# Kernel tuning notes

Measured on AMD Instinct MI355X. Metric: run time of the kernel, lower is better.

The kernel has to match this reference:

```python
import jax, jax.numpy as jnp
import numpy as np

B, S, HID = 2, 2048, 2048
NH, NKV, D = 32, 8, 64
M = 256          # FAVOR+ random features
CHUNK = 128      # causal chunk size
EPS = 1e-6


def setup_inputs():
    key = jax.random.key(0)
    ks = jax.random.split(key, 7)
    hidden_states = jax.random.normal(ks[0], (B, S, HID), jnp.float32)
    # RoPE tables (HF Llama style): [B, S, D]
    inv_freq = 1.0 / (10000.0 ** (jnp.arange(0, D, 2, dtype=jnp.float32) / D))
    freqs = jnp.arange(S, dtype=jnp.float32)[:, None] * inv_freq[None, :]   # [S, D/2]
    emb = jnp.concatenate([freqs, freqs], axis=-1)                          # [S, D]
    cos = jnp.broadcast_to(jnp.cos(emb)[None], (B, S, D)).astype(jnp.float32)
    sin = jnp.broadcast_to(jnp.sin(emb)[None], (B, S, D)).astype(jnp.float32)
    sc = 0.02
    Wq = jax.random.normal(ks[1], (NH * D, HID), jnp.float32) * sc
    Wk = jax.random.normal(ks[2], (NKV * D, HID), jnp.float32) * sc
    Wv = jax.random.normal(ks[3], (NKV * D, HID), jnp.float32) * sc
    Wo = jax.random.normal(ks[4], (HID, NH * D), jnp.float32) * sc
    proj = jax.random.normal(ks[5], (M, D), jnp.float32)  # FAVOR+ random projection
    return {"hidden_states": hidden_states, "cos": cos, "sin": sin,
            "Wq": Wq, "Wk": Wk, "Wv": Wv, "Wo": Wo, "proj": proj}


def rotate_half(x):
    x1, x2 = x[..., : x.shape[-1] // 2], x[..., x.shape[-1] // 2:]
    return jnp.concatenate([-x2, x1], axis=-1)


def favor_features(x, proj, is_query):
    # FAVOR+ positive softmax-kernel features: phi(x) = exp(Wx' - |x'|^2/2 - stab)/sqrt(m)
    dn = x.shape[-1] ** -0.25
    xn = x * dn                                            # data normalizer d^{-1/4}
    xp = jnp.einsum('bhsd,md->bhsm', xn, proj)             # [B,H,S,M]
    sq = 0.5 * jnp.sum(xn * xn, axis=-1, keepdims=True)
    if is_query:
        stab = jnp.max(xp, axis=-1, keepdims=True)
    else:
        stab = jnp.max(xp, axis=(-1, -2), keepdims=True)
    return (jnp.exp(xp - sq - stab) + EPS) / jnp.sqrt(jnp.asarray(M, xp.dtype))


def causal_linear_attention(phi_q, phi_k, v):
    # phi_q/phi_k: [B,H,S,M], v: [B,H,S,D]; causal chunked prefix formulation
    Bh, H, T, m = phi_q.shape
    d = v.shape[-1]
    nc = T // CHUNK
    qc = phi_q.reshape(Bh, H, nc, CHUNK, m)
    kc = phi_k.reshape(Bh, H, nc, CHUNK, m)
    vc = v.reshape(Bh, H, nc, CHUNK, d)
    # per-chunk KV state and key sums
    kv = jnp.einsum('bhscm,bhscd->bhsmd', kc, vc)          # [B,H,nc,M,D]
    kz = jnp.sum(kc, axis=3)                               # [B,H,nc,M]
    kv_pre = jnp.cumsum(kv, axis=2) - kv                   # exclusive prefix
    kz_pre = jnp.cumsum(kz, axis=2) - kz
    inter = jnp.einsum('bhscm,bhsmd->bhscd', qc, kv_pre)
    inter_z = jnp.einsum('bhscm,bhsm->bhsc', qc, kz_pre)
    # intra-chunk causal part
    mask = jnp.tril(jnp.ones((CHUNK, CHUNK), phi_q.dtype))
    scores = jnp.einsum('bhscm,bhstm->bhsct', qc, kc) * mask
    intra = jnp.einsum('bhsct,bhstd->bhscd', scores, vc)
    intra_z = jnp.sum(scores, axis=-1)
    out = (inter + intra) / (inter_z + intra_z + EPS)[..., None]
    return out.reshape(Bh, H, T, d)


def reference(hidden_states, cos, sin, Wq, Wk, Wv, Wo, proj):
    b, s, _ = hidden_states.shape
    q = (hidden_states @ Wq.T).reshape(b, s, NH, D).transpose(0, 2, 1, 3)   # [B,NH,S,D]
    k = (hidden_states @ Wk.T).reshape(b, s, NKV, D).transpose(0, 2, 1, 3)  # [B,NKV,S,D]
    v = (hidden_states @ Wv.T).reshape(b, s, NKV, D).transpose(0, 2, 1, 3)
    c, si = cos[:, None, :, :], sin[:, None, :, :]
    q = q * c + rotate_half(q) * si
    k = k * c + rotate_half(k) * si
    groups = NH // NKV
    k = jnp.repeat(k, groups, axis=1)
    v = jnp.repeat(v, groups, axis=1)
    phi_q = favor_features(q, proj, is_query=True)
    phi_k = favor_features(k, proj, is_query=False)
    attn = causal_linear_attention(phi_q, phi_k, v)                         # [B,NH,S,D]
    attn = attn.transpose(0, 2, 1, 3).reshape(b, s, NH * D)
    return attn @ Wo.T
```

## Files before the change

kernel.cpp:

```cpp
#include <hip/hip_runtime.h>
#include <hip/hip_bf16.h>

#define SEQ   2048
#define NHEAD 32
#define NKVH  8
#define DH    64
#define MFEAT 256
#define NCH   16
#define EPSF  1e-6f

typedef __hip_bfloat16 bf16;
typedef unsigned short u16;
typedef __attribute__((ext_vector_type(8))) short short8;
typedef __attribute__((ext_vector_type(4))) float f32x4;

__device__ __forceinline__ float b2f(bf16 x){ return __bfloat162float(x); }
__device__ __forceinline__ bf16  f2b(float x){ return __float2bfloat16(x); }
__device__ __forceinline__ u16   f2u(float x){ bf16 h = __float2bfloat16(x); return *reinterpret_cast<u16*>(&h); }

__device__ __forceinline__ bool probe_f32(const unsigned* __restrict__ p){
  return (p[0] & 0xFFFFu) == 0u;
}
__device__ __forceinline__ float loadIn(const void* __restrict__ ptr, size_t idx, bool f32){
  return f32 ? ((const float*)ptr)[idx] : b2f(((const bf16*)ptr)[idx]);
}

__device__ __forceinline__ void cp16(u16* lds, const u16* g){
  __builtin_amdgcn_global_load_lds((const __attribute__((address_space(1))) unsigned*)g,
      (__attribute__((address_space(3))) unsigned*)lds, 16, 0, 0);
}

#define MFMA16(a,b,c) __builtin_amdgcn_mfma_f32_16x16x32_bf16(a,b,c,0,0,0)
#define SBAR()  do { __builtin_amdgcn_s_barrier(); __builtin_amdgcn_sched_barrier(0); } while(0)

__global__ __launch_bounds__(256) void conv_kernel(const void* __restrict__ src,
    u16* __restrict__ dst, const unsigned* __restrict__ probe)
{
  const bool f32in = probe_f32(probe);
  size_t i = (size_t)blockIdx.x*256 + threadIdx.x;
  if (f32in){
    const float4* s = (const float4*)src;
    float4 a = s[i*2], b = s[i*2+1];
    u16 t[8] = {f2u(a.x),f2u(a.y),f2u(a.z),f2u(a.w),
                f2u(b.x),f2u(b.y),f2u(b.z),f2u(b.w)};
    *(short8*)&dst[i*8] = *(const short8*)t;
  } else {
    ((short8*)dst)[i] = ((const short8*)src)[i];
  }
}

__global__ __launch_bounds__(512) void gemm_mfma(const u16* __restrict__ A,
    const u16* __restrict__ W, float* __restrict__ oq, float* __restrict__ ok,
    float* __restrict__ ov, void* __restrict__ outAny, int K, int N, int mode,
    const void* __restrict__ cosg, const void* __restrict__ sing,
    const unsigned* __restrict__ probe)
{
  __shared__ __align__(16) u16 sA[3][16384];
  __shared__ __align__(16) u16 sB[3][8192];
  const int tid = threadIdx.x;
  const int lane = tid & 63, wave = tid >> 6;

  const int nbx = gridDim.x;
  const int nwg = nbx * gridDim.y;
  int id = blockIdx.y * nbx + blockIdx.x;
  int sw = id;
  if ((nwg & 7) == 0) sw = (id & 7) * (nwg >> 3) + (id >> 3);
  const int bx = sw % nbx, by = sw / nbx;
  const int c0 = bx*128, r0 = by*256;

  const int wm = wave >> 1, wn = wave & 1;
  f32x4 acc[4][4] = {};

  const int rl  = lane >> 3;
  const int swzE = ((lane & 7) ^ rl) << 3;
  const u16* gA = A + (size_t)(r0 + wave*8 + rl)*K + swzE;
  const u16* gB = W + (size_t)(c0 + wave*8 + rl)*K + swzE;
  const int aDst = wave*512;
  const int bDst = wave*512;

  const int rowA = (wm*64 + (lane&15))*64;
  const int rowB = (wn*64 + (lane&15))*64;
  const int colS = (((lane>>4)*8) ^ ((lane&7)<<3));

  const int nk = K >> 6;

  #define STAGE_ALL(buf, t) do { const int k0_ = (t)*64;                  \
    cp16(&sA[buf][aDst],         gA + k0_);                               \
    cp16(&sA[buf][aDst + 4096],  gA + (size_t)64*K  + k0_);               \
    cp16(&sA[buf][aDst + 8192],  gA + (size_t)128*K + k0_);               \
    cp16(&sA[buf][aDst + 12288], gA + (size_t)192*K + k0_);               \
    cp16(&sB[buf][bDst],         gB + k0_);                               \
    cp16(&sB[buf][bDst + 4096],  gB + (size_t)64*K  + k0_); } while(0)

  STAGE_ALL(0, 0);
  STAGE_ALL(1, 1);

  int cur = 0;
  for (int t = 0; t < nk; ++t) {
    if (t < nk-1) asm volatile("s_waitcnt vmcnt(6)" ::: "memory");
    else          asm volatile("s_waitcnt vmcnt(0)" ::: "memory");
    SBAR();

    int sb = cur + 2; if (sb >= 3) sb -= 3;
    const int k0s = (t + 2) * 64;
    const bool st = (t + 2 < nk);
    const u16* bA_ = sA[cur];
    const u16* bB_ = sB[cur];

    short8 a01[2][2], a23[2][2], b01[2][2], b23[2][2];

    #pragma unroll
    for (int mt=0;mt<2;++mt){
      a01[mt][0] = *(const short8*)(bA_ + rowA + mt*1024 + colS);
      a01[mt][1] = *(const short8*)(bA_ + rowA + mt*1024 + (colS^32));
    }
    #pragma unroll
    for (int nt=0;nt<2;++nt){
      b01[nt][0] = *(const short8*)(bB_ + rowB + nt*1024 + colS);
      b01[nt][1] = *(const short8*)(bB_ + rowB + nt*1024 + (colS^32));
    }
    if (st){ cp16(&sA[sb][aDst], gA + k0s);
             cp16(&sA[sb][aDst + 4096], gA + (size_t)64*K + k0s); }
    SBAR();
    __builtin_amdgcn_s_setprio(1);
    #pragma unroll
    for (int mt=0;mt<2;++mt)
      #pragma unroll
      for (int nt=0;nt<2;++nt){
        acc[mt][nt] = MFMA16(a01[mt][0], b01[nt][0], acc[mt][nt]);
        acc[mt][nt] = MFMA16(a01[mt][1], b01[nt][1], acc[mt][nt]);
      }
    __builtin_amdgcn_s_setprio(0);
    SBAR();

    #pragma unroll
    for (int nt=0;nt<2;++nt){
      b23[nt][0] = *(const short8*)(bB_ + rowB + (nt+2)*1024 + colS);
      b23[nt][1] = *(const short8*)(bB_ + rowB + (nt+2)*1024 + (colS^32));
    }
    if (st){ cp16(&sA[sb][aDst + 8192],  gA + (size_t)128*K + k0s);
             cp16(&sA[sb][aDst + 12288], gA + (size_t)192*K + k0s); }
    SBAR();
    __builtin_amdgcn_s_setprio(1);
    #pragma unroll
    for (int mt=0;mt<2;++mt)
      #pragma unroll
      for (int nt=0;nt<2;++nt){
        acc[mt][nt+2] = MFMA16(a01[mt][0], b23[nt][0], acc[mt][nt+2]);
        acc[mt][nt+2] = MFMA16(a01[mt][1], b23[nt][1], acc[mt][nt+2]);
      }
    __builtin_amdgcn_s_setprio(0);
    SBAR();

    #pragma unroll
    for (int mt=0;mt<2;++mt){
      a23[mt][0] = *(const short8*)(bA_ + rowA + (mt+2)*1024 + colS);
      a23[mt][1] = *(const short8*)(bA_ + rowA + (mt+2)*1024 + (colS^32));
    }
    if (st){ cp16(&sB[sb][bDst], gB + k0s);
             cp16(&sB[sb][bDst + 4096], gB + (size_t)64*K + k0s); }
    SBAR();
    __builtin_amdgcn_s_setprio(1);
    #pragma unroll
    for (int mt=0;mt<2;++mt)
      #pragma unroll
      for (int nt=0;nt<2;++nt){
        acc[mt+2][nt+2] = MFMA16(a23[mt][0], b23[nt][0], acc[mt+2][nt+2]);
        acc[mt+2][nt+2] = MFMA16(a23[mt][1], b23[nt][1], acc[mt+2][nt+2]);
      }
    __builtin_amdgcn_s_setprio(0);
    SBAR();

    __builtin_amdgcn_s_setprio(1);
    #pragma unroll
    for (int mt=0;mt<2;++mt)
      #pragma unroll
      for (int nt=0;nt<2;++nt){
        acc[mt+2][nt] = MFMA16(a23[mt][0], b01[nt][0], acc[mt+2][nt]);
        acc[mt+2][nt] = MFMA16(a23[mt][1], b01[nt][1], acc[mt+2][nt]);
      }
    __builtin_amdgcn_s_setprio(0);

    cur = (cur == 2) ? 0 : cur + 1;
  }
  #undef STAGE_ALL

  const int rbase = r0 + wm*64 + (lane>>4)*4;
  const int cbase = c0 + wn*64 + (lane&15);
  if (mode == 0) {
    const bool f32o = probe_f32(probe);
    #pragma unroll
    for (int mt=0;mt<4;++mt)
      #pragma unroll
      for (int nt=0;nt<4;++nt)
        #pragma unroll
        for (int rg=0;rg<4;++rg){
          int r = rbase + mt*16 + rg, c = cbase + nt*16;
          float v = acc[mt][nt][rg];
          if (f32o) ((float*)outAny)[(size_t)r*N + c] = v;
          else      ((u16*)outAny)[(size_t)r*N + c] = f2u(v);
        }
  } else {
    const bool f32in = probe_f32(probe);
    const float dn = 0.3535533905932738f;
    #pragma unroll
    for (int nt=0;nt<4;++nt){
      int cc = cbase + nt*16;
      float* dst; int H2, cl; bool isv = false;
      if (cc < 2048){ dst = oq; H2 = 32; cl = cc; }
      else if (cc < 2560){ dst = ok; H2 = 8; cl = cc - 2048; }
      else { dst = ov; H2 = 8; cl = cc - 2560; isv = true; }
      int hh = cl>>6, dd = cl&63;
      float sgn = (dd < 32) ? -1.f : 1.f;
      #pragma unroll
      for (int mt=0;mt<4;++mt)
        #pragma unroll
        for (int rg=0;rg<4;++rg){
          int r = rbase + mt*16 + rg;
          int bb = r>>11, s = r&2047;
          float v = acc[mt][nt][rg];
          if (!isv){
            float vp = acc[mt][nt^2][rg];
            size_t ci = ((size_t)bb*SEQ + s)*DH + dd;
            float cv = loadIn(cosg, ci, f32in);
            float sv = loadIn(sing, ci, f32in);
            v = (v*cv + sgn*vp*sv) * dn;
          }
          dst[(((size_t)bb*H2 + hh)*SEQ + s)*DH + dd] = v;
        }
    }
  }
}

__global__ __launch_bounds__(256) void phi_mfma(const float* __restrict__ xn,
    const u16* __restrict__ projb, float* __restrict__ rmaxk,
    const float* __restrict__ stabk, u16* __restrict__ phi, int mode)
{
  __shared__ __align__(16) u16 sA[64*80];
  __shared__ __align__(16) u16 sP[256*80];
  __shared__ float sq[64];
  const int tid = threadIdx.x, lane = tid & 63, wave = tid >> 6;
  const size_t row0 = (size_t)blockIdx.x * 64;

  #pragma unroll
  for (int l = 0; l < 8; ++l){
    int v8 = tid + l*256;
    int off = v8*8; int m = off>>6, d = off&63;
    *(short8*)&sP[m*80 + d] = ((const short8*)projb)[v8];
  }
  {
    int r = tid >> 2, qq = tid & 3;
    const float* src = xn + (row0 + r)*DH + qq*16;
    float s = 0.f;
    u16 tmp[16];
    #pragma unroll
    for (int i=0;i<16;i+=4){
      float4 v4 = *(const float4*)&src[i];
      s += v4.x*v4.x + v4.y*v4.y + v4.z*v4.z + v4.w*v4.w;
      tmp[i] = f2u(v4.x); tmp[i+1] = f2u(v4.y); tmp[i+2] = f2u(v4.z); tmp[i+3] = f2u(v4.w);
    }
    *(short8*)&sA[r*80 + qq*16]     = *(short8*)&tmp[0];
    *(short8*)&sA[r*80 + qq*16 + 8] = *(short8*)&tmp[8];
    s += __shfl_xor(s, 1, 64);
    s += __shfl_xor(s, 2, 64);
    if (qq == 0) sq[r] = 0.5f*s;
  }
  __syncthreads();

  f32x4 acc[16] = {};
  const u16* pA = &sA[(wave*16 + (lane&15))*80 + (lane>>4)*8];
  short8 af0 = *(const short8*)(pA);
  short8 af1 = *(const short8*)(pA + 32);
  #pragma unroll
  for (int nt=0; nt<16; ++nt){
    const u16* pB = &sP[(nt*16 + (lane&15))*80 + (lane>>4)*8];
    short8 b0 = *(const short8*)(pB);
    short8 b1 = *(const short8*)(pB + 32);
    acc[nt] = MFMA16(af0, b0, acc[nt]);
    acc[nt] = MFMA16(af1, b1, acc[nt]);
  }

  float mx[4];
  #pragma unroll
  for (int rg=0; rg<4; ++rg){
    float m = acc[0][rg];
    #pragma unroll
    for (int nt=1; nt<16; ++nt) m = fmaxf(m, acc[nt][rg]);
    m = fmaxf(m, __shfl_xor(m, 1, 64));
    m = fmaxf(m, __shfl_xor(m, 2, 64));
    m = fmaxf(m, __shfl_xor(m, 4, 64));
    m = fmaxf(m, __shfl_xor(m, 8, 64));
    mx[rg] = m;
  }
  const int rloc = wave*16 + (lane>>4)*4;
  if (mode == 1){
    if ((lane & 15) == 0){
      #pragma unroll
      for (int rg=0;rg<4;++rg) rmaxk[row0 + rloc + rg] = mx[rg];
    }
    return;
  }
  float stab[4];
  if (mode == 0){
    #pragma unroll
    for (int rg=0;rg<4;++rg) stab[rg] = mx[rg];
  } else {
    float s = stabk[row0 >> 11];
    #pragma unroll
    for (int rg=0;rg<4;++rg) stab[rg] = s;
  }
  float sqr[4];
  #pragma unroll
  for (int rg=0;rg<4;++rg) sqr[rg] = sq[rloc + rg];
  #pragma unroll
  for (int nt=0;nt<16;++nt){
    #pragma unroll
    for (int rg=0;rg<4;++rg){
      float val = (__expf(fminf(acc[nt][rg] - sqr[rg] - stab[rg], 0.f)) + EPSF) * 0.0625f;
      phi[(row0 + rloc + rg)*MFEAT + nt*16 + (lane&15)] = f2u(val);
    }
  }
}

__global__ void stab_reduce_kernel(const float* __restrict__ rmaxk, float* __restrict__ stabk){
  __shared__ float red[256];
  int bk = blockIdx.x;
  float mx = -1e30f;
  for (int i = threadIdx.x; i < SEQ; i += 256) mx = fmaxf(mx, rmaxk[(size_t)bk*SEQ + i]);
  red[threadIdx.x] = mx; __syncthreads();
  for (int off=128; off>0; off>>=1){
    if ((int)threadIdx.x < off) red[threadIdx.x] = fmaxf(red[threadIdx.x], red[threadIdx.x+off]);
    __syncthreads();
  }
  if (threadIdx.x==0) stabk[bk] = red[0];
}

__global__ __launch_bounds__(256) void vtrans_kernel(const float* __restrict__ vbuf,
                                                     u16* __restrict__ vT)
{
  int blk = blockIdx.x;
  int bk = blk >> 4, sc = blk & 15;
  const float* src = vbuf + ((size_t)bk*SEQ + sc*128)*DH;
  __shared__ float sT[128*65];
  for (int i=0;i<32;++i){ int idx = threadIdx.x + i*256; sT[(idx>>6)*65 + (idx&63)] = src[idx]; }
  __syncthreads();
  #pragma unroll
  for (int i=0;i<4;++i){
    int gi = threadIdx.x + i*256;
    int d = gi >> 4, t8 = (gi & 15)*8;
    u16 tmp[8];
    #pragma unroll
    for (int j=0;j<8;++j) tmp[j] = f2u(sT[(t8+j)*65 + d]);
    *(short8*)&vT[((size_t)bk*DH + d)*SEQ + sc*128 + t8] = *(const short8*)tmp;
  }
}

__global__ __launch_bounds__(256) void kvchunk_kernel(const bf16* __restrict__ phik,
    const float* __restrict__ vbuf, float* __restrict__ kv, float* __restrict__ kz)
{
  int blk = blockIdx.x; int bk = blk >> 4, c = blk & 15;
  const bf16* Kc = phik + ((size_t)bk*SEQ + c*128)*MFEAT;
  const float* Vc = vbuf + ((size_t)bk*SEQ + c*128)*DH;
  __shared__ float sV[128*64];
  for (int l=0;l<32;++l){ int idx = threadIdx.x + l*256; sV[idx] = Vc[idx]; }
  __syncthreads();
  int m = threadIdx.x;
  float acc[64] = {}; float az = 0.f;
  for (int t=0;t<128;++t){
    float ph = b2f(Kc[(size_t)t*MFEAT + m]);
    az += ph;
    const float4* vr = (const float4*)&sV[t*64];
    #pragma unroll
    for (int d4=0; d4<16; ++d4){
      float4 v4 = vr[d4];
      acc[d4*4+0] += ph*v4.x; acc[d4*4+1] += ph*v4.y;
      acc[d4*4+2] += ph*v4.z; acc[d4*4+3] += ph*v4.w;
    }
  }
  float* out = kv + (size_t)blk*MFEAT*DH;
  #pragma unroll
  for (int d=0; d<64; ++d) out[(size_t)d*MFEAT + m] = acc[d];
  kz[(size_t)blk*MFEAT + m] = az;
}

__global__ void scan_kernel(float* __restrict__ p, u16* __restrict__ ob,
                            int inner, int nc, int total){
  int t = blockIdx.x*256 + threadIdx.x;
  if (t >= total) return;
  int outer = t / inner, rem = t - outer*inner;
  const float* base = p + (size_t)outer*nc*inner + rem;
  u16* obase = ob + (size_t)outer*nc*inner + rem;
  float run = 0.f;
  for (int c=0;c<nc;++c){
    float v = base[(size_t)c*inner];
    obase[(size_t)c*inner] = f2u(run);
    run += v;
  }
}

__global__ __launch_bounds__(256) void attn_mfma(
    const u16* __restrict__ phiq, const u16* __restrict__ phik,
    const u16* __restrict__ kvpb, const u16* __restrict__ kzpb,
    const u16* __restrict__ vT, u16* __restrict__ attnout)
{
  __shared__ __align__(16) u16 smem[27648];
  __shared__ float sZ[128];
  const int tid = threadIdx.x, lane = tid & 63, wave = tid >> 6;
  const int blk = blockIdx.x;
  const int c = blk & 15, h = (blk >> 4) & 31, b = blk >> 9;
  const int kvh = h >> 2;
  const int bkv = b*NKVH + kvh;
  const u16* Q   = phiq + (((size_t)(b*NHEAD+h)*SEQ) + c*128)*MFEAT;
  const u16* Kc  = phik + (((size_t)bkv*SEQ) + c*128)*MFEAT;
  const u16* KVb = kvpb + ((size_t)(bkv*NCH + c))*MFEAT*DH;
  const u16* KZb = kzpb + ((size_t)(bkv*NCH + c))*MFEAT;
  const u16* vTb = vT + (size_t)bkv*DH*SEQ;

  u16* sQ   = smem;
  u16* sK   = smem + 4096;
  u16* sKVT = smem + 8192;
  u16* sP   = smem;
  u16* sVT  = smem + 17408;

  f32x4 accS[2][8] = {};
  f32x4 accO[2][5] = {};

  #pragma unroll
  for (int i=0;i<4;++i){
    int gi = tid + i*256;
    int d  = gi >> 4, g = gi & 15;
    cp16(&sVT[(i*256 + wave*64)*8],
         vTb + (size_t)d*SEQ + c*128 + ((g ^ (d&7))<<3));
  }

  const int ch0 = wave*64 + lane, ch1 = 256 + wave*64 + lane;
  const u16* gQ0 = Q  + (ch0>>2)*MFEAT + (ch0&3)*8;
  const u16* gQ1 = Q  + (ch1>>2)*MFEAT + (ch1&3)*8;
  const u16* gK0 = Kc + (ch0>>2)*MFEAT + (ch0&3)*8;
  const u16* gK1 = Kc + (ch1>>2)*MFEAT + (ch1&3)*8;
  u16* lQ0 = &sQ[(wave*64)*8];  u16* lQ1 = &sQ[(256+wave*64)*8];
  u16* lK0 = &sK[(wave*64)*8];  u16* lK1 = &sK[(256+wave*64)*8];

  const int dKV = wave*16 + (lane>>2);
  const u16* gKVsrc = KVb + (size_t)dKV*MFEAT + (((lane&3) ^ (dKV&3))<<3);

  for (int k0 = 0; k0 < MFEAT; k0 += 32) {
    cp16(lQ0, gQ0 + k0); cp16(lQ1, gQ1 + k0);
    cp16(lK0, gK0 + k0); cp16(lK1, gK1 + k0);
    cp16(&sKVT[wave*512], gKVsrc + k0);
    if (tid < 4) cp16(&sKVT[2048], KZb + k0 + tid*8);
    __syncthreads();
    short8 af0, af1;
    const u16* pQ = &sQ[(wave*32 + (lane&15))*32 + (lane>>4)*8];
    af0 = *(const short8*)(pQ);
    af1 = *(const short8*)(pQ + 512);
    #pragma unroll
    for (int nt=0;nt<8;++nt){
      short8 bk = *(const short8*)&sK[(nt*16 + (lane&15))*32 + (lane>>4)*8];
      accS[0][nt] = MFMA16(af0, bk, accS[0][nt]);
      accS[1][nt] = MFMA16(af1, bk, accS[1][nt]);
    }
    #pragma unroll
    for (int nt=0;nt<5;++nt){
      int row = nt*16 + (lane&15);
      short8 bi = *(const short8*)&sKVT[row*32 + (((lane>>4) ^ (row&3))<<3)];
      accO[0][nt] = MFMA16(af0, bi, accO[0][nt]);
      accO[1][nt] = MFMA16(af1, bi, accO[1][nt]);
    }
    __syncthreads();
  }

  #pragma unroll
  for (int mt=0;mt<2;++mt){
    int rowb = wave*32 + mt*16 + (lane>>4)*4;
    #pragma unroll
    for (int nt=0;nt<8;++nt){
      int col = nt*16 + (lane&15);
      #pragma unroll
      for (int rg=0;rg<4;++rg){
        int row = rowb + rg;
        float v = (col <= row) ? accS[mt][nt][rg] : 0.f;
        sP[row*136 + col] = f2u(v);
      }
    }
  }
  if (tid < 16){
    u16 ones[8] = {0x3F80,0x3F80,0x3F80,0x3F80,0x3F80,0x3F80,0x3F80,0x3F80};
    *(short8*)&sVT[64*128 + tid*8] = *(const short8*)ones;
  }
  __syncthreads();

  #pragma unroll
  for (int kc=0;kc<4;++kc){
    const u16* pP = &sP[(wave*32 + (lane&15))*136 + kc*32 + (lane>>4)*8];
    short8 pa0 = *(const short8*)(pP);
    short8 pa1 = *(const short8*)(pP + 16*136);
    #pragma unroll
    for (int nt=0;nt<5;++nt){
      int row = nt*16 + (lane&15);
      int g   = kc*4 + (lane>>4);
      short8 bv = *(const short8*)&sVT[row*128 + ((g ^ (row&7))<<3)];
      accO[0][nt] = MFMA16(pa0, bv, accO[0][nt]);
      accO[1][nt] = MFMA16(pa1, bv, accO[1][nt]);
    }
  }

  if ((lane & 15) == 0){
    #pragma unroll
    for (int mt=0;mt<2;++mt){
      int rowb = wave*32 + mt*16 + (lane>>4)*4;
      #pragma unroll
      for (int rg=0;rg<4;++rg) sZ[rowb + rg] = accO[mt][4][rg];
    }
  }
  __syncthreads();
  const int d0 = lane & 15;
  #pragma unroll
  for (int mt=0;mt<2;++mt){
    int rowb = wave*32 + mt*16 + (lane>>4)*4;
    #pragma unroll
    for (int rg=0;rg<4;++rg){
      int row = rowb + rg;
      float inv = 1.0f / (sZ[row] + EPSF);
      int sg = c*128 + row;
      size_t ob = (((size_t)b*SEQ + sg)*NHEAD + h)*DH;
      #pragma unroll
      for (int nt=0;nt<4;++nt)
        attnout[ob + nt*16 + d0] = f2u(accO[mt][nt][rg] * inv);
    }
  }
}

extern "C" void kernel_launch(void* const* d_in, const int* in_sizes, int n_in,
                              void* d_out, int out_size, void* d_ws, size_t ws_size,
                              hipStream_t stream)
{
  const void* hidden = d_in[0];
  const void* cosg   = d_in[1];
  const void* sing   = d_in[2];
  const void* Wq     = d_in[3];
  const void* Wk     = d_in[4];
  const void* Wv     = d_in[5];
  const void* Wo     = d_in[6];
  const void* proj   = d_in[7];
  const unsigned* probe = (const unsigned*)d_in[1];

  float* ws = (float*)d_ws;
  float* xnq   = ws;
  float* kv    = ws;
  float* kz    = ws + 4194304;
  float* rmaxk = ws + 4259840;
  float* stabk = ws + 4292608;
  u16*   vT    = (u16*) (ws + 4292864);
  u16*   kvpb  = (u16*) (ws + 5341440);
  u16*   kzpb  = (u16*) (ws + 7438592);
  float* xnk   = ws + 8388608;
  float* vbuf  = ws + 10485760;
  u16*   projb = (u16*) (ws + 12582912);
  bf16*  phiq  = (bf16*)(ws + 12591104);
  bf16*  phik  = (bf16*)(ws + 29368320);
  u16*   hb    = (u16*) (ws + 33562624);
  u16*   attn  = (u16*) (ws + 33562624);
  u16*   wqkv  = (u16*) (ws + 37756928);
  u16*   wob   = (u16*) (ws + 37756928);

  conv_kernel<<<4096, 256, 0, stream>>>(hidden, hb, probe);
  conv_kernel<<<2048, 256, 0, stream>>>(Wq, wqkv,           probe);
  conv_kernel<<<512,  256, 0, stream>>>(Wk, wqkv + 4194304, probe);
  conv_kernel<<<512,  256, 0, stream>>>(Wv, wqkv + 5242880, probe);
  conv_kernel<<<8,    256, 0, stream>>>(proj, projb, probe);

  gemm_mfma<<<dim3(24,16), 512, 0, stream>>>(hb, wqkv, xnq, xnk, vbuf, nullptr,
                                             2048, 3072, 1, cosg, sing, probe);
  conv_kernel<<<2048, 256, 0, stream>>>(Wo, wob, probe);

  phi_mfma<<<2048, 256, 0, stream>>>(xnq, projb, nullptr, nullptr, (u16*)phiq, 0);
  vtrans_kernel<<<256, 256, 0, stream>>>(vbuf, vT);
  phi_mfma<<<512,  256, 0, stream>>>(xnk, projb, rmaxk, nullptr, nullptr, 1);
  stab_reduce_kernel<<<16, 256, 0, stream>>>(rmaxk, stabk);
  phi_mfma<<<512,  256, 0, stream>>>(xnk, projb, nullptr, stabk, (u16*)phik, 2);

  kvchunk_kernel<<<256, 256, 0, stream>>>(phik, vbuf, kv, kz);
  scan_kernel<<<1024, 256, 0, stream>>>(kv, kvpb, MFEAT*DH, NCH, 16*MFEAT*DH);
  scan_kernel<<<16,   256, 0, stream>>>(kz, kzpb, MFEAT,    NCH, 16*MFEAT);

  attn_mfma<<<1024, 256, 0, stream>>>((const u16*)phiq, (const u16*)phik,
                                      kvpb, kzpb, vT, attn);

  gemm_mfma<<<dim3(16,16), 512, 0, stream>>>(attn, wob, nullptr, nullptr, nullptr,
                                             d_out, 2048, 2048, 0, nullptr, nullptr, probe);
}
```

Baseline: 441.7 us.

## Double-buffer attention operand loads and coalesce feature-map stores via LDS

The attention kernel now double-buffers the Q, K and KV/KZ shared-memory tiles. The next 32-wide slice is prefetched with async copies while MFMAs run on the current slice, using explicit vmcnt waits and one barrier per step. Separately, the FAVOR feature kernel stages its exp outputs in a swizzled shared buffer and writes them to global memory as 16-byte coalesced vectors instead of scattered 2-byte stores. This raises LDS use per block, which may lower occupancy, and adds extra barriers to the feature kernel.

```diff
diff --git a/kernel.cpp b/kernel.cpp
--- a/kernel.cpp
+++ b/kernel.cpp
@@ -312,13 +312,27 @@
   float sqr[4];
   #pragma unroll
   for (int rg=0;rg<4;++rg) sqr[rg] = sq[rloc + rg];
+
+  __syncthreads();
+  u16* sOut = sP;
+  const int xorW = (lane>>4) << 2;
   #pragma unroll
   for (int nt=0;nt<16;++nt){
+    int gcol = nt*2 + ((lane&15)>>3);
+    int gS = (gcol ^ xorW)*8 + (lane&7);
     #pragma unroll
     for (int rg=0;rg<4;++rg){
       float val = (__expf(fminf(acc[nt][rg] - sqr[rg] - stab[rg], 0.f)) + EPSF) * 0.0625f;
-      phi[(row0 + rloc + rg)*MFEAT + nt*16 + (lane&15)] = f2u(val);
-    }
+      sOut[(rloc + rg)*256 + gS] = f2u(val);
+    }
+  }
+  __syncthreads();
+  #pragma unroll
+  for (int j=0;j<8;++j){
+    int idx = tid + j*256;
+    int r = idx >> 5, g = idx & 31;
+    short8 v = *(const short8*)&sOut[r*256 + (g ^ (((r>>2)&3)<<2))*8];
+    *(short8*)&phi[(row0 + r)*MFEAT + g*8] = v;
   }
 }
 
@@ -403,7 +417,7 @@
     const u16* __restrict__ kvpb, const u16* __restrict__ kzpb,
     const u16* __restrict__ vT, u16* __restrict__ attnout)
 {
-  __shared__ __align__(16) u16 smem[27648];
+  __shared__ __align__(16) u16 smem[31232];
   __shared__ float sZ[128];
   const int tid = threadIdx.x, lane = tid & 63, wave = tid >> 6;
   const int blk = blockIdx.x;
@@ -416,15 +430,34 @@
   const u16* KZb = kzpb + ((size_t)(bkv*NCH + c))*MFEAT;
   const u16* vTb = vT + (size_t)bkv*DH*SEQ;
 
-  u16* sQ   = smem;
-  u16* sK   = smem + 4096;
-  u16* sKVT = smem + 8192;
-  u16* sP   = smem;
-  u16* sVT  = smem + 17408;
+  u16* sQb[2]  = { smem,         smem + 4096 };
+  u16* sKb[2]  = { smem + 8192,  smem + 12288 };
+  u16* sKVb[2] = { smem + 16384, smem + 18560 };
+  u16* sVT = smem + 20736;
+  u16* sP  = smem;
 
   f32x4 accS[2][8] = {};
   f32x4 accO[2][5] = {};
 
+  const int ch0 = wave*64 + lane, ch1 = 256 + wave*64 + lane;
+  const u16* gQ0 = Q  + (ch0>>2)*MFEAT + (ch0&3)*8;
+  const u16* gQ1 = Q  + (ch1>>2)*MFEAT + (ch1&3)*8;
+  const u16* gK0 = Kc + (ch0>>2)*MFEAT + (ch0&3)*8;
+  const u16* gK1 = Kc + (ch1>>2)*MFEAT + (ch1&3)*8;
+
+  const int dKV = wave*16 + (lane>>2);
+  const u16* gKVsrc = KVb + (size_t)dKV*MFEAT + (((lane&3) ^ (dKV&3))<<3);
+
+  #define ASTAGE(bi, kk) do {                                      \
+    cp16(sQb[bi] + wave*512,        gQ0 + (kk));                   \
+    cp16(sQb[bi] + 2048 + wave*512, gQ1 + (kk));                   \
+    cp16(sKb[bi] + wave*512,        gK0 + (kk));                   \
+    cp16(sKb[bi] + 2048 + wave*512, gK1 + (kk));                   \
+    cp16(sKVb[bi] + wave*512,       gKVsrc + (kk));                \
+    if (tid < 4) cp16(sKVb[bi] + 2048, KZb + (kk) + tid*8);        \
+  } while(0)
+
+  ASTAGE(0, 0);
   #pragma unroll
   for (int i=0;i<4;++i){
     int gi = tid + i*256;
@@ -432,43 +465,35 @@
     cp16(&sVT[(i*256 + wave*64)*8],
          vTb + (size_t)d*SEQ + c*128 + ((g ^ (d&7))<<3));
   }
-
-  const int ch0 = wave*64 + lane, ch1 = 256 + wave*64 + lane;
-  const u16* gQ0 = Q  + (ch0>>2)*MFEAT + (ch0&3)*8;
-  const u16* gQ1 = Q  + (ch1>>2)*MFEAT + (ch1&3)*8;
-  const u16* gK0 = Kc + (ch0>>2)*MFEAT + (ch0&3)*8;
-  const u16* gK1 = Kc + (ch1>>2)*MFEAT + (ch1&3)*8;
-  u16* lQ0 = &sQ[(wave*64)*8];  u16* lQ1 = &sQ[(256+wave*64)*8];
-  u16* lK0 = &sK[(wave*64)*8];  u16* lK1 = &sK[(256+wave*64)*8];
-
-  const int dKV = wave*16 + (lane>>2);
-  const u16* gKVsrc = KVb + (size_t)dKV*MFEAT + (((lane&3) ^ (dKV&3))<<3);
-
-  for (int k0 = 0; k0 < MFEAT; k0 += 32) {
-    cp16(lQ0, gQ0 + k0); cp16(lQ1, gQ1 + k0);
-    cp16(lK0, gK0 + k0); cp16(lK1, gK1 + k0);
-    cp16(&sKVT[wave*512], gKVsrc + k0);
-    if (tid < 4) cp16(&sKVT[2048], KZb + k0 + tid*8);
-    __syncthreads();
+  asm volatile("s_waitcnt vmcnt(4)" ::: "memory");
+  SBAR();
+
+  #pragma unroll
+  for (int t = 0; t < 8; ++t) {
+    const int bi = t & 1;
+    if (t < 7) ASTAGE(bi^1, (t+1)*32);
+
     short8 af0, af1;
-    const u16* pQ = &sQ[(wave*32 + (lane&15))*32 + (lane>>4)*8];
+    const u16* pQ = &sQb[bi][(wave*32 + (lane&15))*32 + (lane>>4)*8];
     af0 = *(const short8*)(pQ);
     af1 = *(const short8*)(pQ + 512);
     #pragma unroll
     for (int nt=0;nt<8;++nt){
-      short8 bk = *(const short8*)&sK[(nt*16 + (lane&15))*32 + (lane>>4)*8];
+      short8 bk = *(const short8*)&sKb[bi][(nt*16 + (lane&15))*32 + (lane>>4)*8];
       accS[0][nt] = MFMA16(af0, bk, accS[0][nt]);
       accS[1][nt] = MFMA16(af1, bk, accS[1][nt]);
     }
     #pragma unroll
     for (int nt=0;nt<5;++nt){
       int row = nt*16 + (lane&15);
-      short8 bi = *(const short8*)&sKVT[row*32 + (((lane>>4) ^ (row&3))<<3)];
-      accO[0][nt] = MFMA16(af0, bi, accO[0][nt]);
-      accO[1][nt] = MFMA16(af1, bi, accO[1][nt]);
-    }
-    __syncthreads();
-  }
+      short8 bi8 = *(const short8*)&sKVb[bi][row*32 + (((lane>>4) ^ (row&3))<<3)];
+      accO[0][nt] = MFMA16(af0, bi8, accO[0][nt]);
+      accO[1][nt] = MFMA16(af1, bi8, accO[1][nt]);
+    }
+    asm volatile("s_waitcnt vmcnt(0)" ::: "memory");
+    SBAR();
+  }
+  #undef ASTAGE
 
   #pragma unroll
   for (int mt=0;mt<2;++mt){
```

Measured after the change: 446.4 us. No clear change (+1.1%).
